# Kernel optimization log

Measured on AMD Instinct MI355X. Metric: run time of the kernel, lower is better.

The kernel has to match this reference:

```python
import jax, jax.numpy as jnp
import numpy as np

B, S, HID = 2, 2048, 1024
NH, HD = 4, 256
SCALE = HD ** -0.5


def _rope(x, fr, fi):
    # x: [B,S,NH,HD]; fr/fi: [S,HD//2]
    b, s, n, d = x.shape
    xr = x.reshape(b, s, n, d // 2, 2)
    re, im = xr[..., 0], xr[..., 1]
    fr = fr[None, :, None, :]
    fi = fi[None, :, None, :]
    rr = re * fr - im * fi
    ri = re * fi + im * fr
    return jnp.stack((rr, ri), axis=-1).reshape(b, s, n, d)


def setup_inputs() -> dict:
    key = jax.random.key(0)
    k1, k2, k3 = jax.random.split(key, 3)
    hidden_states = jax.random.normal(k1, (B, S, HID), dtype=jnp.float32)
    # RoPE frequencies (standard theta=10000)
    inv_freq = 1.0 / (10000.0 ** (np.arange(0, HD, 2, dtype=np.float32) / HD))  # [HD//2]
    t = np.arange(S, dtype=np.float32)
    ang = np.outer(t, inv_freq)  # [S, HD//2]
    freqs_real = jnp.asarray(np.cos(ang), dtype=jnp.float32)
    freqs_imag = jnp.asarray(np.sin(ang), dtype=jnp.float32)
    # causal additive mask [1,1,S,S]
    causal = jnp.tril(jnp.ones((S, S), dtype=bool))
    mask = jnp.where(causal, 0.0, -1e9).astype(jnp.float32)[None, None]
    W_qkv = jax.random.normal(k2, (3 * HID, HID), dtype=jnp.float32) * (HID ** -0.5)
    W_o = jax.random.normal(k3, (HID, HID), dtype=jnp.float32) * (HID ** -0.5)
    return {"hidden_states": hidden_states, "freqs_real": freqs_real,
            "freqs_imag": freqs_imag, "mask": mask, "W_qkv": W_qkv, "W_o": W_o}


def reference(hidden_states, freqs_real, freqs_imag, mask, W_qkv, W_o):
    b, s, _ = hidden_states.shape
    qkv = hidden_states @ W_qkv.T  # [B,S,3*HID]
    qkv = qkv.reshape(b, s, 3, NH, HD)
    q, k, v = qkv[:, :, 0], qkv[:, :, 1], qkv[:, :, 2]
    q = _rope(q, freqs_real, freqs_imag)
    k = _rope(k, freqs_real, freqs_imag)
    scores = jnp.einsum('bqhd,bkhd->bhqk', q * SCALE, k) + mask  # [B,NH,S,S]
    probs = jax.nn.softmax(scores, axis=-1)
    attn = jnp.einsum('bhqk,bkhd->bqhd', probs, v).reshape(b, s, HID)
    return attn @ W_o.T
```

## Files before the change

kernel.cpp:

```cpp
#include <hip/hip_runtime.h>
#include <stdint.h>

#define NB 2
#define NS 2048
#define NHID 1024
#define NHEADS 4
#define DHEAD 256
#define NP 128
#define QK_SCALE 0.0625f

typedef unsigned short ushort_t;
typedef __bf16 bf16x8 __attribute__((ext_vector_type(8)));
typedef float floatx4 __attribute__((ext_vector_type(4)));
typedef short shortx8 __attribute__((ext_vector_type(8)));
typedef unsigned short ushortx4 __attribute__((ext_vector_type(4)));
typedef unsigned short ushortx8 __attribute__((ext_vector_type(8)));

__device__ __forceinline__ float bf2f(ushort_t u) {
    unsigned int x = ((unsigned int)u) << 16;
    return __builtin_bit_cast(float, x);
}
__device__ __forceinline__ ushort_t f2bf(float f) {
    unsigned int u = __builtin_bit_cast(unsigned int, f);
    u += 0x7fff + ((u >> 16) & 1);
    return (ushort_t)(u >> 16);
}

__device__ __forceinline__ floatx4 mfma16(bf16x8 a, bf16x8 b, floatx4 c) {
    return __builtin_amdgcn_mfma_f32_16x16x32_bf16(a, b, c, 0, 0, 0);
}

__device__ __forceinline__ void gload_lds16(const void* g, void* l) {
    __builtin_amdgcn_global_load_lds(
        (const __attribute__((address_space(1))) void*)g,
        (__attribute__((address_space(3))) void*)l, 16, 0, 0);
}

#define N4_H (4096 * 1024 / 4)
#define N4_WQ (3072 * 1024 / 4)
#define N4_WO (1024 * 1024 / 4)
__global__ __launch_bounds__(256) void cast3_kernel(const float* __restrict__ inH,
                                                    const float* __restrict__ inWq,
                                                    const float* __restrict__ inWo,
                                                    ushort_t* __restrict__ out) {
    int i = blockIdx.x * 256 + threadIdx.x;
    const float* src;
    int j = i;
    if (i < N4_H) {
        src = inH;
    } else if (i < N4_H + N4_WQ) {
        src = inWq; j = i - N4_H;
    } else {
        src = inWo; j = i - (N4_H + N4_WQ);
    }
    float4 v = ((const float4*)src)[j];
    ushortx4 o = { f2bf(v.x), f2bf(v.y), f2bf(v.z), f2bf(v.w) };
    ((ushortx4*)out)[i] = o;
}

__global__ __launch_bounds__(256) void gemm_bt_f32s(const ushort_t* __restrict__ A,
                                                    const ushort_t* __restrict__ Bt,
                                                    float* __restrict__ C0,
                                                    float* __restrict__ C1,
                                                    int M, int N, int K) {
    __shared__ ushort_t sA[4][128 * 32];
    __shared__ ushort_t sB[4][128 * 32];
    const int t = threadIdx.x;
    const int f = blockIdx.x;
    const int xcd = f & 7;
    const int idx = f >> 3;
    const int im = idx >> 4;
    const int in = (idx >> 1) & 7;
    const int kz = idx & 1;
    const int m0 = (xcd * 4 + im) * 128;
    const int n0 = in * 128;
    float* Cout = kz ? C1 : C0;
    const int kbeg = kz * (K / 2);
    const int w = t >> 6, l = t & 63;
    const int wm = (w >> 1) * 64, wn = (w & 1) * 64;
    const int lc = l & 15, lq = l >> 4;

    floatx4 acc[4][4];
#pragma unroll
    for (int i = 0; i < 4; i++)
#pragma unroll
        for (int j = 0; j < 4; j++) acc[i][j] = (floatx4){0.f, 0.f, 0.f, 0.f};

    const int srow = w * 16 + (l >> 2);
    const int scol = (((l & 3) - (l >> 2) - (l >> 4)) & 3) * 8;
    const ushort_t* Ag = A + (size_t)(m0 + srow) * K + scol + kbeg;
    const ushort_t* Bg = Bt + (size_t)(n0 + srow) * K + scol + kbeg;
    const int lofs = t * 8;

    auto stage = [&](int bsel, int kk) {
        ushort_t* lA = &sA[bsel][lofs];
        ushort_t* lB = &sB[bsel][lofs];
        gload_lds16(Ag + kk, lA);
        gload_lds16(Ag + kk + (size_t)64 * K, lA + 2048);
        gload_lds16(Bg + kk, lB);
        gload_lds16(Bg + kk + (size_t)64 * K, lB + 2048);
    };
    auto compute = [&](int bsel) {
        const ushort_t* cA = sA[bsel];
        const ushort_t* cB = sB[bsel];
        bf16x8 af[4], bfv[4];
#pragma unroll
        for (int i = 0; i < 4; i++) {
            int R = wm + i * 16 + lc;
            af[i] = *(const bf16x8*)&cA[R * 32 + ((lq + R + (R >> 2)) & 3) * 8];
        }
#pragma unroll
        for (int j = 0; j < 4; j++) {
            int R = wn + j * 16 + lc;
            bfv[j] = *(const bf16x8*)&cB[R * 32 + ((lq + R + (R >> 2)) & 3) * 8];
        }
#pragma unroll
        for (int i = 0; i < 4; i++)
#pragma unroll
            for (int j = 0; j < 4; j++)
                acc[i][j] = mfma16(af[i], bfv[j], acc[i][j]);
    };

    stage(0, 0); stage(1, 32); stage(2, 64);
#pragma unroll 1
    for (int s = 0; s <= 16 - 4; ++s) {
        asm volatile("s_waitcnt vmcnt(8)" ::: "memory");
        __builtin_amdgcn_sched_barrier(0);
        __builtin_amdgcn_s_barrier();
        asm volatile("" ::: "memory");
        compute(s & 3);
        stage((s + 3) & 3, (s + 3) * 32);
    }
    asm volatile("s_waitcnt vmcnt(8)" ::: "memory");
    __builtin_amdgcn_sched_barrier(0);
    __builtin_amdgcn_s_barrier();
    asm volatile("" ::: "memory");
    compute(13 & 3);
    asm volatile("s_waitcnt vmcnt(4)" ::: "memory");
    __builtin_amdgcn_sched_barrier(0);
    __builtin_amdgcn_s_barrier();
    asm volatile("" ::: "memory");
    compute(14 & 3);
    asm volatile("s_waitcnt vmcnt(0)" ::: "memory");
    __builtin_amdgcn_sched_barrier(0);
    __builtin_amdgcn_s_barrier();
    asm volatile("" ::: "memory");
    compute(15 & 3);

#pragma unroll
    for (int i = 0; i < 4; i++) {
        int row = m0 + wm + i * 16 + lq * 4;
#pragma unroll
        for (int j = 0; j < 4; j++) {
            int col = n0 + wn + j * 16 + lc;
#pragma unroll
            for (int r = 0; r < 4; r++)
                Cout[(size_t)(row + r) * N + col] = acc[i][j][r];
        }
    }
}

__global__ __launch_bounds__(256) void add_f32(const float* __restrict__ a,
                                               const float* __restrict__ b,
                                               float* __restrict__ o, int n4) {
    int i = blockIdx.x * 256 + threadIdx.x;
    if (i < n4) {
        float4 x = ((const float4*)a)[i];
        float4 y = ((const float4*)b)[i];
        float4 z = { x.x + y.x, x.y + y.y, x.z + y.z, x.w + y.w };
        ((float4*)o)[i] = z;
    }
}

__global__ __launch_bounds__(512, 2) void gemm_qkv(const ushort_t* __restrict__ A,
                                                   const ushort_t* __restrict__ Bt,
                                                   const float* __restrict__ fre,
                                                   const float* __restrict__ fim,
                                                   ushort_t* __restrict__ Q,
                                                   ushort_t* __restrict__ Kk,
                                                   ushort_t* __restrict__ Vt) {
    __shared__ ushort_t sA[2][16384];
    __shared__ ushort_t sB[2][12288];
    const int t = threadIdx.x;
    const int f = blockIdx.x;
    const int xcd = f & 7;
    const int idx = f >> 3;
    const int mreg = xcd >> 1, nreg = xcd & 1;
    const int im = idx & 3, in = idx >> 2;
    const int m0 = (mreg * 4 + im) * 256;
    const int n0 = (nreg * 8 + in) * 192;
    const int w = t >> 6, l = t & 63;
    const int wr = w >> 2, wc = w & 3;
    const int wrm = wr * 128, wcn = wc * 48;
    const int lc = l & 15, lq = l >> 4;

    floatx4 acc[8][3];
#pragma unroll
    for (int i = 0; i < 8; i++)
#pragma unroll
        for (int j = 0; j < 3; j++) acc[i][j] = (floatx4){0.f, 0.f, 0.f, 0.f};

    const int arow = t >> 3;
    const int ac8 = ((((t & 7) - (arow & 7)) & 7)) * 8;
    const ushort_t* Ab = A + (size_t)(m0 + arow) * 1024 + ac8;
    const ushort_t* Bb = Bt + (size_t)(n0 + arow) * 1024 + ac8;
    const int ldst = t * 8;

    auto STAGE_A2 = [&](int buf, int half, int kk) {
        gload_lds16(Ab + (size_t)(half * 128) * 1024 + kk, &sA[buf][half * 8192 + ldst]);
        gload_lds16(Ab + (size_t)(half * 128 + 64) * 1024 + kk, &sA[buf][half * 8192 + 4096 + ldst]);
    };
    auto STAGE_B3 = [&](int buf, int kk) {
        gload_lds16(Bb + kk, &sB[buf][ldst]);
        gload_lds16(Bb + (size_t)64 * 1024 + kk, &sB[buf][4096 + ldst]);
        gload_lds16(Bb + (size_t)128 * 1024 + kk, &sB[buf][8192 + ldst]);
    };

#define QWAITV0  do { asm volatile("s_waitcnt vmcnt(0)" ::: "memory"); \
                      __builtin_amdgcn_sched_barrier(0); } while (0)
#define QWAITL   do { asm volatile("s_waitcnt lgkmcnt(0)" ::: "memory"); \
                      __builtin_amdgcn_sched_barrier(0); } while (0)
#define QBAR     do { asm volatile("" ::: "memory"); \
                      __builtin_amdgcn_s_barrier(); \
                      asm volatile("" ::: "memory"); } while (0)

    STAGE_A2(0, 0, 0); STAGE_A2(0, 1, 0); STAGE_B3(0, 0);

#pragma unroll 1
    for (int kt = 0; kt < 16; ++kt) {
        const int b = kt & 1, nb = b ^ 1;
        const int kn = (kt + 1) * 64;
        const ushort_t* cA = sA[b];
        const ushort_t* cB = sB[b];
        bf16x8 af[4][2], bfr[3][2];

        QWAITV0;
        QBAR;
#pragma unroll
        for (int ii = 0; ii < 4; ii++) {
            const int R = wrm + ii * 16 + lc;
            af[ii][0] = *(const bf16x8*)&cA[R * 64 + ((lq + R) & 7) * 8];
            af[ii][1] = *(const bf16x8*)&cA[R * 64 + ((4 + lq + R) & 7) * 8];
        }
#pragma unroll
        for (int jj = 0; jj < 2; jj++) {
            const int R = wcn + jj * 16 + lc;
            bfr[jj][0] = *(const bf16x8*)&cB[R * 64 + ((lq + R) & 7) * 8];
            bfr[jj][1] = *(const bf16x8*)&cB[R * 64 + ((4 + lq + R) & 7) * 8];
        }
        if (kt < 15) STAGE_A2(nb, 0, kn);
        QWAITL;
        __builtin_amdgcn_s_setprio(1);
#pragma unroll
        for (int ii = 0; ii < 4; ii++)
#pragma unroll
            for (int jj = 0; jj < 2; jj++) {
                acc[ii][jj] = mfma16(af[ii][0], bfr[jj][0], acc[ii][jj]);
                acc[ii][jj] = mfma16(af[ii][1], bfr[jj][1], acc[ii][jj]);
            }
        __builtin_amdgcn_s_setprio(0);

        QBAR;
        {
            const int R = wcn + 32 + lc;
            bfr[2][0] = *(const bf16x8*)&cB[R * 64 + ((lq + R) & 7) * 8];
            bfr[2][1] = *(const bf16x8*)&cB[R * 64 + ((4 + lq + R) & 7) * 8];
        }
        if (kt < 15) STAGE_A2(nb, 1, kn);
        QWAITL;
        __builtin_amdgcn_s_setprio(1);
#pragma unroll
        for (int ii = 0; ii < 4; ii++) {
            acc[ii][2] = mfma16(af[ii][0], bfr[2][0], acc[ii][2]);
            acc[ii][2] = mfma16(af[ii][1], bfr[2][1], acc[ii][2]);
        }
        __builtin_amdgcn_s_setprio(0);

        QBAR;
#pragma unroll
        for (int ii = 0; ii < 4; ii++) {
            const int R = wrm + 64 + ii * 16 + lc;
            af[ii][0] = *(const bf16x8*)&cA[R * 64 + ((lq + R) & 7) * 8];
            af[ii][1] = *(const bf16x8*)&cA[R * 64 + ((4 + lq + R) & 7) * 8];
        }
        if (kt < 15) STAGE_B3(nb, kn);
        QWAITL;
        __builtin_amdgcn_s_setprio(1);
#pragma unroll
        for (int ii = 0; ii < 4; ii++) {
            acc[4 + ii][2] = mfma16(af[ii][0], bfr[2][0], acc[4 + ii][2]);
            acc[4 + ii][2] = mfma16(af[ii][1], bfr[2][1], acc[4 + ii][2]);
        }
        __builtin_amdgcn_s_setprio(0);

        QBAR;
#pragma unroll
        for (int jj = 0; jj < 2; jj++) {
            const int R = wcn + jj * 16 + lc;
            bfr[jj][0] = *(const bf16x8*)&cB[R * 64 + ((lq + R) & 7) * 8];
            bfr[jj][1] = *(const bf16x8*)&cB[R * 64 + ((4 + lq + R) & 7) * 8];
        }
        QWAITL;
        __builtin_amdgcn_s_setprio(1);
#pragma unroll
        for (int ii = 0; ii < 4; ii++)
#pragma unroll
            for (int jj = 0; jj < 2; jj++) {
                acc[4 + ii][jj] = mfma16(af[ii][0], bfr[jj][0], acc[4 + ii][jj]);
                acc[4 + ii][jj] = mfma16(af[ii][1], bfr[jj][1], acc[4 + ii][jj]);
            }
        __builtin_amdgcn_s_setprio(0);
    }

#pragma unroll
    for (int i = 0; i < 8; i++) {
        int row = m0 + wrm + i * 16 + lq * 4;
        int bb = row >> 11;
        int srow2 = row & 2047;
#pragma unroll
        for (int j = 0; j < 3; j++) {
            int c0 = n0 + wcn + j * 16;
            int sect = c0 >> 10;
            int h = (c0 >> 8) & 3;
            int d = (c0 & 255) + lc;
            int bh = bb * NHEADS + h;
            if (sect == 2) {
                ushortx4 pack = { f2bf(acc[i][j][0]), f2bf(acc[i][j][1]),
                                  f2bf(acc[i][j][2]), f2bf(acc[i][j][3]) };
                *(ushortx4*)&Vt[((size_t)bh * 256 + d) * NS + srow2] = pack;
            } else {
                int p = d >> 1;
                int odd = d & 1;
                ushort_t* dst = (sect == 0) ? Q : Kk;
#pragma unroll
                for (int r = 0; r < 4; r++) {
                    float v = acc[i][j][r];
                    float vp = __shfl_xor(v, 1);
                    int s = srow2 + r;
                    float c = fre[s * NP + p], si = fim[s * NP + p];
                    float out = odd ? (vp * si + v * c) : (v * c - vp * si);
                    if (sect == 0) out *= QK_SCALE;
                    dst[((size_t)bh * NS + s) * DHEAD + d] = f2bf(out);
                }
            }
        }
    }
}

#define BQ3 128
#define BKV3 64
#define PPAD 72
#define CHCAP 6
#define NPART_BH 51
#define OPART_SPLIT 224

__global__ __launch_bounds__(256, 2) void flash_attn4(const ushort_t* __restrict__ Q,
                                                      const ushort_t* __restrict__ K,
                                                      const ushort_t* __restrict__ Vt,
                                                      ushort_t* __restrict__ OpA,
                                                      ushort_t* __restrict__ OpB,
                                                      float* __restrict__ ml) {
    __shared__ ushort_t sK[BKV3 * 256];
    __shared__ ushort_t sV[DHEAD * 64];
    __shared__ ushort_t sP[4][16 * PPAD];

    int rem = blockIdx.x, qt = 15, nsp;
    for (;;) {
        nsp = (2 * (qt + 1) + CHCAP - 1) / CHCAP;
        if (rem < nsp) break;
        rem -= nsp;
        qt--;
    }
    const int nch = 2 * (qt + 1);
    const int cbeg = rem * CHCAP;
    const int cend = (cbeg + CHCAP < nch) ? cbeg + CHCAP : nch;

    const int h = blockIdx.y, b = blockIdx.z;
    const int t = threadIdx.x, w = t >> 6, l = t & 63;
    const int lc = l & 15, lq = l >> 4;
    const int bh = b * NHEADS + h;
    const size_t base = (size_t)bh * NS * DHEAD;
    const int q0 = qt * BQ3;

    const int krb = w * 2 + (l >> 5);
    const int kck = ((l & 31) - (krb & 7)) & 31;
    const size_t koff = (size_t)krb * 256 + kck * 8;
    const int vrb = w * 8 + (l >> 3);
    const int vck = ((l & 7) - (vrb & 7)) & 7;
    const size_t voff = (size_t)vrb * NS + vck * 8;
    ushort_t* dK = &sK[w * 512 + l * 8];
    ushort_t* dV = &sV[w * 512 + l * 8];

    bf16x8 qf[2][8];
#pragma unroll
    for (int gq = 0; gq < 2; gq++) {
        const ushort_t* qrow = Q + base + (size_t)(q0 + w * 32 + gq * 16 + lc) * DHEAD + lq * 8;
#pragma unroll
        for (int dk = 0; dk < 8; dk++) qf[gq][dk] = *(const bf16x8*)(qrow + dk * 32);
    }

    floatx4 accO[2][16];
#pragma unroll
    for (int gq = 0; gq < 2; gq++)
#pragma unroll
        for (int j = 0; j < 16; j++) accO[gq][j] = (floatx4){0.f, 0.f, 0.f, 0.f};
    float lrun[2][4] = {{0.f, 0.f, 0.f, 0.f}, {0.f, 0.f, 0.f, 0.f}};

    for (int kc = cbeg; kc < cend; kc++) {
        const int kb = kc * BKV3;
        __syncthreads();
        {
            const ushort_t* ksrc = K + base + (size_t)kb * 256 + koff;
            const ushort_t* vsrc = Vt + base + kb + voff;
#pragma unroll
            for (int j = 0; j < 8; j++)
                gload_lds16(ksrc + j * (8 * 256), dK + j * 2048);
#pragma unroll
            for (int j = 0; j < 8; j++)
                gload_lds16(vsrc + j * (32 * NS), dV + j * 2048);
        }
        __syncthreads();

        floatx4 sfr[2][4];
#pragma unroll
        for (int gq = 0; gq < 2; gq++)
#pragma unroll
            for (int g = 0; g < 4; g++) sfr[gq][g] = (floatx4){0.f, 0.f, 0.f, 0.f};
#pragma unroll
        for (int dk = 0; dk < 8; dk++) {
#pragma unroll
            for (int g = 0; g < 4; g++) {
                int R = g * 16 + lc;
                int phys = (dk * 4 + lq + (R & 7)) & 31;
                bf16x8 bk = *(const bf16x8*)&sK[R * 256 + phys * 8];
                sfr[0][g] = mfma16(qf[0][dk], bk, sfr[0][g]);
                sfr[1][g] = mfma16(qf[1][dk], bk, sfr[1][g]);
            }
        }

        if (kc >= nch - 2) {
#pragma unroll
            for (int gq = 0; gq < 2; gq++)
#pragma unroll
                for (int g = 0; g < 4; g++) {
                    int kg = kb + g * 16 + lc;
                    int qr = q0 + w * 32 + gq * 16 + lq * 4;
#pragma unroll
                    for (int r = 0; r < 4; r++)
                        if (kg > qr + r) sfr[gq][g][r] = -1e30f;
                }
        }

        ushort_t* pw = sP[w];
#pragma unroll
        for (int gq = 0; gq < 2; gq++) {
#pragma unroll
            for (int g = 0; g < 4; g++)
#pragma unroll
                for (int r = 0; r < 4; r++) {
                    float p = __expf(sfr[gq][g][r]);
                    lrun[gq][r] += p;
                    pw[(lq * 4 + r) * PPAD + g * 16 + lc] = f2bf(p);
                }
            bf16x8 ap0 = *(const bf16x8*)&pw[lc * PPAD + lq * 8];
            bf16x8 ap1 = *(const bf16x8*)&pw[lc * PPAD + 32 + lq * 8];
#pragma unroll
            for (int j = 0; j < 16; j++) {
                int D = j * 16 + lc;
                int ph0 = (lq + (D & 7)) & 7;
                int ph1 = (4 + lq + (D & 7)) & 7;
                bf16x8 bv0 = *(const bf16x8*)&sV[D * 64 + ph0 * 8];
                bf16x8 bv1 = *(const bf16x8*)&sV[D * 64 + ph1 * 8];
                accO[gq][j] = mfma16(ap0, bv0, accO[gq][j]);
                accO[gq][j] = mfma16(ap1, bv1, accO[gq][j]);
            }
        }
    }

    const int pid = bh * NPART_BH + blockIdx.x;
    ushort_t* op = (pid < OPART_SPLIT) ? OpA + (size_t)pid * (128 * 256)
                                       : OpB + (size_t)(pid - OPART_SPLIT) * (128 * 256);
#pragma unroll
    for (int gq = 0; gq < 2; gq++) {
#pragma unroll
        for (int r = 0; r < 4; r++) {
            int row = w * 32 + gq * 16 + lq * 4 + r;
#pragma unroll
            for (int j = 0; j < 16; j++)
                op[row * 256 + j * 16 + lc] = f2bf(accO[gq][j][r]);
            float lv = lrun[gq][r];
#pragma unroll
            for (int off = 1; off < 16; off <<= 1) lv += __shfl_xor(lv, off);
            if (lc == 0) ml[(size_t)pid * 128 + row] = lv;
        }
    }
}

__global__ __launch_bounds__(256) void combine_parts2(const ushort_t* __restrict__ OpA,
                                                      const ushort_t* __restrict__ OpB,
                                                      const float* __restrict__ ml,
                                                      ushort_t* __restrict__ O) {
    const int qt = blockIdx.x >> 3, rsub = blockIdx.x & 7;
    const int h = blockIdx.y, b = blockIdx.z;
    const int bh = b * NHEADS + h;
    int bbase = 0;
    for (int q = 15; q > qt; q--) bbase += (2 * (q + 1) + CHCAP - 1) / CHCAP;
    const int nsp = (2 * (qt + 1) + CHCAP - 1) / CHCAP;
    const int pid0 = bh * NPART_BH + bbase;

    const int t = threadIdx.x;
    const int rl = t >> 4;
    const int c0 = (t & 15) * 16;
    const int row = rsub * 16 + rl;

    float so[16];
#pragma unroll
    for (int k = 0; k < 16; k++) so[k] = 0.f;
    float sl = 0.f;

    for (int i = 0; i < nsp; i++) {
        int pid = pid0 + i;
        const ushort_t* op = (pid < OPART_SPLIT)
                                 ? OpA + (size_t)pid * (128 * 256)
                                 : OpB + (size_t)(pid - OPART_SPLIT) * (128 * 256);
        const ushort_t* p = op + row * 256 + c0;
        ushortx8 a0 = *(const ushortx8*)p;
        ushortx8 a1 = *(const ushortx8*)(p + 8);
#pragma unroll
        for (int k = 0; k < 8; k++) {
            so[k] += bf2f(a0[k]);
            so[8 + k] += bf2f(a1[k]);
        }
        sl += ml[(size_t)pid * 128 + row];
    }

    float inv = 1.f / sl;
    ushortx8 o0, o1;
#pragma unroll
    for (int k = 0; k < 8; k++) {
        o0[k] = f2bf(so[k] * inv);
        o1[k] = f2bf(so[8 + k] * inv);
    }
    int s = qt * BQ3 + row;
    ushort_t* dst = O + ((size_t)(b * NS + s) * NHEADS + h) * DHEAD + c0;
    *(ushortx8*)dst = o0;
    *(ushortx8*)(dst + 8) = o1;
}

extern "C" void kernel_launch(void* const* d_in, const int* in_sizes, int n_in,
                              void* d_out, int out_size, void* d_ws, size_t ws_size,
                              hipStream_t stream) {
    const float* hidden = (const float*)d_in[0];
    const float* fre = (const float*)d_in[1];
    const float* fim = (const float*)d_in[2];
    const float* Wqkv = (const float*)d_in[4];
    const float* Wo = (const float*)d_in[5];

    char* ws = (char*)d_ws;
    ushort_t* hb    = (ushort_t*)(ws);
    ushort_t* wqkvb = (ushort_t*)(ws + 8388608);
    ushort_t* wob   = (ushort_t*)(ws + 14680064);
    ushort_t* qb    = (ushort_t*)(ws + 16777216);
    ushort_t* kb    = (ushort_t*)(ws + 25165824);
    ushort_t* vtb   = (ushort_t*)(ws + 33554432);
    ushort_t* OpA   = (ushort_t*)(ws);
    ushort_t* OpB   = (ushort_t*)(ws + 41943040);
    ushort_t* oattn = (ushort_t*)(ws + 16777216);
    float*    gP0   = (float*)(ws + 25165824);
    float*    gP1   = (float*)(ws + 41943040);
    float*    ml    = (float*)(ws + 58720256);

    cast3_kernel<<<(N4_H + N4_WQ + N4_WO) / 256, 256, 0, stream>>>(hidden, Wqkv, Wo, hb);

    gemm_qkv<<<dim3(256), 512, 0, stream>>>(
        hb, wqkvb, fre, fim, qb, kb, vtb);

    flash_attn4<<<dim3(NPART_BH, NHEADS, NB), 256, 0, stream>>>(qb, kb, vtb, OpA, OpB, ml);
    combine_parts2<<<dim3(128, NHEADS, NB), 256, 0, stream>>>(OpA, OpB, ml, oattn);

    gemm_bt_f32s<<<dim3(512), 256, 0, stream>>>(
        oattn, wob, gP0, gP1, 4096, 1024, 1024);
    add_f32<<<4096, 256, 0, stream>>>(gP0, gP1, (float*)d_out, 4096 * 1024 / 4);
}
```

Before: 200.5 us.

## Drop split-K in output GEMM and split K/V load waits in attention

The output projection GEMM no longer splits K in two halves writing partial buffers that a separate add kernel sums. It now uses 128x64 tiles over the full K with double-buffered 64-wide K stages, priority boosts around the MFMA block, and writes directly to the output. This removes the extra add kernel and the partial-sum traffic. In flash attention, the single syncthreads after issuing K and V loads becomes a wait on the K loads only, plus a later wait for V, so the V load overlaps the QK^T MFMAs. The GEMM now has a less deep pipeline and per-block work is reshaped, which may cost some latency hiding.

```diff
diff --git a/kernel.cpp b/kernel.cpp
--- a/kernel.cpp
+++ b/kernel.cpp
@@ -35,6 +35,16 @@
         (const __attribute__((address_space(1))) void*)g,
         (__attribute__((address_space(3))) void*)l, 16, 0, 0);
 }
+
+#define QWAITV0  do { asm volatile("s_waitcnt vmcnt(0)" ::: "memory"); \
+                      __builtin_amdgcn_sched_barrier(0); } while (0)
+#define QWAITV8  do { asm volatile("s_waitcnt vmcnt(8)" ::: "memory"); \
+                      __builtin_amdgcn_sched_barrier(0); } while (0)
+#define QWAITL   do { asm volatile("s_waitcnt lgkmcnt(0)" ::: "memory"); \
+                      __builtin_amdgcn_sched_barrier(0); } while (0)
+#define QBAR     do { asm volatile("" ::: "memory"); \
+                      __builtin_amdgcn_s_barrier(); \
+                      asm volatile("" ::: "memory"); } while (0)
 
 #define N4_H (4096 * 1024 / 4)
 #define N4_WQ (3072 * 1024 / 4)
@@ -58,117 +68,93 @@
     ((ushortx4*)out)[i] = o;
 }
 
-__global__ __launch_bounds__(256) void gemm_bt_f32s(const ushort_t* __restrict__ A,
-                                                    const ushort_t* __restrict__ Bt,
-                                                    float* __restrict__ C0,
-                                                    float* __restrict__ C1,
-                                                    int M, int N, int K) {
-    __shared__ ushort_t sA[4][128 * 32];
-    __shared__ ushort_t sB[4][128 * 32];
+__global__ __launch_bounds__(256, 2) void gemm_bt_f32s(const ushort_t* __restrict__ A,
+                                                       const ushort_t* __restrict__ Bt,
+                                                       float* __restrict__ C,
+                                                       int M, int N, int K) {
+    __shared__ ushort_t sA[2][8192];
+    __shared__ ushort_t sB[2][4096];
     const int t = threadIdx.x;
     const int f = blockIdx.x;
     const int xcd = f & 7;
     const int idx = f >> 3;
-    const int im = idx >> 4;
-    const int in = (idx >> 1) & 7;
-    const int kz = idx & 1;
-    const int m0 = (xcd * 4 + im) * 128;
-    const int n0 = in * 128;
-    float* Cout = kz ? C1 : C0;
-    const int kbeg = kz * (K / 2);
+    const int m0 = (xcd * 4 + (idx & 3)) * 128;
+    const int n0 = (idx >> 2) * 64;
     const int w = t >> 6, l = t & 63;
-    const int wm = (w >> 1) * 64, wn = (w & 1) * 64;
+    const int wr = w >> 1, wc = w & 1;
+    const int wrm = wr * 64, wcn = wc * 32;
     const int lc = l & 15, lq = l >> 4;
 
-    floatx4 acc[4][4];
+    floatx4 acc[4][2];
 #pragma unroll
     for (int i = 0; i < 4; i++)
 #pragma unroll
-        for (int j = 0; j < 4; j++) acc[i][j] = (floatx4){0.f, 0.f, 0.f, 0.f};
-
-    const int srow = w * 16 + (l >> 2);
-    const int scol = (((l & 3) - (l >> 2) - (l >> 4)) & 3) * 8;
-    const ushort_t* Ag = A + (size_t)(m0 + srow) * K + scol + kbeg;
-    const ushort_t* Bg = Bt + (size_t)(n0 + srow) * K + scol + kbeg;
-    const int lofs = t * 8;
-
-    auto stage = [&](int bsel, int kk) {
-        ushort_t* lA = &sA[bsel][lofs];
-        ushort_t* lB = &sB[bsel][lofs];
-        gload_lds16(Ag + kk, lA);
-        gload_lds16(Ag + kk + (size_t)64 * K, lA + 2048);
-        gload_lds16(Bg + kk, lB);
-        gload_lds16(Bg + kk + (size_t)64 * K, lB + 2048);
+        for (int j = 0; j < 2; j++) acc[i][j] = (floatx4){0.f, 0.f, 0.f, 0.f};
+
+    const int arow = t >> 3;
+    const int ac8 = ((((t & 7) - (arow & 7)) & 7)) * 8;
+    const ushort_t* Ab = A + (size_t)(m0 + arow) * K + ac8;
+    const ushort_t* Bb = Bt + (size_t)(n0 + arow) * K + ac8;
+    const int ldst = t * 8;
+
+    auto STAGE_A = [&](int buf, int kk) {
+#pragma unroll
+        for (int is = 0; is < 4; is++)
+            gload_lds16(Ab + (size_t)(is * 32) * K + kk, &sA[buf][is * 2048 + ldst]);
     };
-    auto compute = [&](int bsel) {
-        const ushort_t* cA = sA[bsel];
-        const ushort_t* cB = sB[bsel];
-        bf16x8 af[4], bfv[4];
-#pragma unroll
-        for (int i = 0; i < 4; i++) {
-            int R = wm + i * 16 + lc;
-            af[i] = *(const bf16x8*)&cA[R * 32 + ((lq + R + (R >> 2)) & 3) * 8];
-        }
-#pragma unroll
-        for (int j = 0; j < 4; j++) {
-            int R = wn + j * 16 + lc;
-            bfv[j] = *(const bf16x8*)&cB[R * 32 + ((lq + R + (R >> 2)) & 3) * 8];
-        }
-#pragma unroll
-        for (int i = 0; i < 4; i++)
-#pragma unroll
-            for (int j = 0; j < 4; j++)
-                acc[i][j] = mfma16(af[i], bfv[j], acc[i][j]);
+    auto STAGE_B = [&](int buf, int kk) {
+#pragma unroll
+        for (int is = 0; is < 2; is++)
+            gload_lds16(Bb + (size_t)(is * 32) * K + kk, &sB[buf][is * 2048 + ldst]);
     };
 
-    stage(0, 0); stage(1, 32); stage(2, 64);
+    STAGE_A(0, 0); STAGE_B(0, 0);
+
 #pragma unroll 1
-    for (int s = 0; s <= 16 - 4; ++s) {
-        asm volatile("s_waitcnt vmcnt(8)" ::: "memory");
-        __builtin_amdgcn_sched_barrier(0);
-        __builtin_amdgcn_s_barrier();
-        asm volatile("" ::: "memory");
-        compute(s & 3);
-        stage((s + 3) & 3, (s + 3) * 32);
-    }
-    asm volatile("s_waitcnt vmcnt(8)" ::: "memory");
-    __builtin_amdgcn_sched_barrier(0);
-    __builtin_amdgcn_s_barrier();
-    asm volatile("" ::: "memory");
-    compute(13 & 3);
-    asm volatile("s_waitcnt vmcnt(4)" ::: "memory");
-    __builtin_amdgcn_sched_barrier(0);
-    __builtin_amdgcn_s_barrier();
-    asm volatile("" ::: "memory");
-    compute(14 & 3);
-    asm volatile("s_waitcnt vmcnt(0)" ::: "memory");
-    __builtin_amdgcn_sched_barrier(0);
-    __builtin_amdgcn_s_barrier();
-    asm volatile("" ::: "memory");
-    compute(15 & 3);
+    for (int kt = 0; kt < 16; ++kt) {
+        const int b = kt & 1, nb = b ^ 1;
+        const int kn = (kt + 1) * 64;
+        const ushort_t* cA = sA[b];
+        const ushort_t* cB = sB[b];
+        bf16x8 af[4][2], bfr[2][2];
+
+        QWAITV0;
+        QBAR;
+#pragma unroll
+        for (int ii = 0; ii < 4; ii++) {
+            const int R = wrm + ii * 16 + lc;
+            af[ii][0] = *(const bf16x8*)&cA[R * 64 + ((lq + R) & 7) * 8];
+            af[ii][1] = *(const bf16x8*)&cA[R * 64 + ((4 + lq + R) & 7) * 8];
+        }
+#pragma unroll
+        for (int jj = 0; jj < 2; jj++) {
+            const int R = wcn + jj * 16 + lc;
+            bfr[jj][0] = *(const bf16x8*)&cB[R * 64 + ((lq + R) & 7) * 8];
+            bfr[jj][1] = *(const bf16x8*)&cB[R * 64 + ((4 + lq + R) & 7) * 8];
+        }
+        if (kt < 15) { STAGE_A(nb, kn); STAGE_B(nb, kn); }
+        QWAITL;
+        __builtin_amdgcn_s_setprio(1);
+#pragma unroll
+        for (int ii = 0; ii < 4; ii++)
+#pragma unroll
+            for (int jj = 0; jj < 2; jj++) {
+                acc[ii][jj] = mfma16(af[ii][0], bfr[jj][0], acc[ii][jj]);
+                acc[ii][jj] = mfma16(af[ii][1], bfr[jj][1], acc[ii][jj]);
+            }
+        __builtin_amdgcn_s_setprio(0);
+    }
 
 #pragma unroll
     for (int i = 0; i < 4; i++) {
-        int row = m0 + wm + i * 16 + lq * 4;
-#pragma unroll
-        for (int j = 0; j < 4; j++) {
-            int col = n0 + wn + j * 16 + lc;
+        int row = m0 + wrm + i * 16 + lq * 4;
+#pragma unroll
+        for (int j = 0; j < 2; j++) {
+            int col = n0 + wcn + j * 16 + lc;
 #pragma unroll
             for (int r = 0; r < 4; r++)
-                Cout[(size_t)(row + r) * N + col] = acc[i][j][r];
-        }
-    }
-}
-
-__global__ __launch_bounds__(256) void add_f32(const float* __restrict__ a,
-                                               const float* __restrict__ b,
-                                               float* __restrict__ o, int n4) {
-    int i = blockIdx.x * 256 + threadIdx.x;
-    if (i < n4) {
-        float4 x = ((const float4*)a)[i];
-        float4 y = ((const float4*)b)[i];
-        float4 z = { x.x + y.x, x.y + y.y, x.z + y.z, x.w + y.w };
-        ((float4*)o)[i] = z;
+                C[(size_t)(row + r) * N + col] = acc[i][j][r];
+        }
     }
 }
 
@@ -216,14 +202,6 @@
         gload_lds16(Bb + (size_t)128 * 1024 + kk, &sB[buf][8192 + ldst]);
     };
 
-#define QWAITV0  do { asm volatile("s_waitcnt vmcnt(0)" ::: "memory"); \
-                      __builtin_amdgcn_sched_barrier(0); } while (0)
-#define QWAITL   do { asm volatile("s_waitcnt lgkmcnt(0)" ::: "memory"); \
-                      __builtin_amdgcn_sched_barrier(0); } while (0)
-#define QBAR     do { asm volatile("" ::: "memory"); \
-                      __builtin_amdgcn_s_barrier(); \
-                      asm volatile("" ::: "memory"); } while (0)
-
     STAGE_A2(0, 0, 0); STAGE_A2(0, 1, 0); STAGE_B3(0, 0);
 
 #pragma unroll 1
@@ -419,7 +397,8 @@
             for (int j = 0; j < 8; j++)
                 gload_lds16(vsrc + j * (32 * NS), dV + j * 2048);
         }
-        __syncthreads();
+        QWAITV8;
+        QBAR;
 
         floatx4 sfr[2][4];
 #pragma unroll
@@ -450,6 +429,9 @@
                         if (kg > qr + r) sfr[gq][g][r] = -1e30f;
                 }
         }
+
+        QWAITV0;
+        QBAR;
 
         ushort_t* pw = sP[w];
 #pragma unroll
@@ -566,8 +548,6 @@
     ushort_t* OpA   = (ushort_t*)(ws);
     ushort_t* OpB   = (ushort_t*)(ws + 41943040);
     ushort_t* oattn = (ushort_t*)(ws + 16777216);
-    float*    gP0   = (float*)(ws + 25165824);
-    float*    gP1   = (float*)(ws + 41943040);
     float*    ml    = (float*)(ws + 58720256);
 
     cast3_kernel<<<(N4_H + N4_WQ + N4_WO) / 256, 256, 0, stream>>>(hidden, Wqkv, Wo, hb);
@@ -579,6 +559,5 @@
     combine_parts2<<<dim3(128, NHEADS, NB), 256, 0, stream>>>(OpA, OpB, ml, oattn);
 
     gemm_bt_f32s<<<dim3(512), 256, 0, stream>>>(
-        oattn, wob, gP0, gP1, 4096, 1024, 1024);
-    add_f32<<<4096, 256, 0, stream>>>(gP0, gP1, (float*)d_out, 4096 * 1024 / 4);
-}
+        oattn, wob, (float*)d_out, 4096, 1024, 1024);
+}
```

After: 191.0 us. 1.05x faster.
